# Kernel tuning notes

Hardware: AMD Instinct MI355X
Metric: run time of the kernel (lower is better)

Reference implementation:

```python
import jax, jax.numpy as jnp
import numpy as np
from jax import lax

DN = ('NCHW', 'OIHW', 'NCHW')

def conv(x, w, b, stride):
    y = lax.conv_general_dilated(x, w, (stride, stride), ((1, 1), (1, 1)), dimension_numbers=DN)
    return y + b[None, :, None, None]

def deconv(x, w, b):
    # PyTorch ConvTranspose2d(k=3, stride=2, padding=1, output_padding=1): doubles H, W.
    # w has torch layout [in, out, kH, kW]; convert to OIHW and flip spatially.
    wt = jnp.flip(w, (-2, -1)).transpose(1, 0, 2, 3)
    y = lax.conv_general_dilated(x, wt, (1, 1), ((1, 2), (1, 2)), lhs_dilation=(2, 2), dimension_numbers=DN)
    return y + b[None, :, None, None]


def setup_inputs() -> dict:
    key = jax.random.key(0)
    ks = jax.random.split(key, 16)
    s = 0.05
    d = {
        'x': jax.random.normal(ks[0], (16, 3, 256, 256), jnp.float32),
        'w1': jax.random.normal(ks[1], (64, 3, 3, 3), jnp.float32) * s,
        'b1': jnp.zeros((64,), jnp.float32),
        'w2': jax.random.normal(ks[2], (128, 64, 3, 3), jnp.float32) * s,
        'b2': jnp.zeros((128,), jnp.float32),
        'w3': jax.random.normal(ks[3], (256, 128, 3, 3), jnp.float32) * s,
        'b3': jnp.zeros((256,), jnp.float32),
        'w4': jax.random.normal(ks[4], (512, 256, 3, 3), jnp.float32) * s,
        'b4': jnp.zeros((512,), jnp.float32),
        'codebook': jax.random.normal(ks[5], (8192, 512), jnp.float32),
        # ConvTranspose2d weights in torch layout [in, out, kH, kW]
        'd1w': jax.random.normal(ks[6], (512, 256, 3, 3), jnp.float32) * s,
        'd1b': jnp.zeros((256,), jnp.float32),
        'd2w': jax.random.normal(ks[7], (256, 128, 3, 3), jnp.float32) * s,
        'd2b': jnp.zeros((128,), jnp.float32),
        'd3w': jax.random.normal(ks[8], (128, 64, 3, 3), jnp.float32) * s,
        'd3b': jnp.zeros((64,), jnp.float32),
        'wo': jax.random.normal(ks[9], (3, 64, 3, 3), jnp.float32) * s,
        'bo': jnp.zeros((3,), jnp.float32),
    }
    return d


def reference(x, w1, b1, w2, b2, w3, b3, w4, b4, codebook, d1w, d1b, d2w, d2b, d3w, d3b, wo, bo):
    # Encoder: 256 -> 256 -> 128 -> 64 -> 32 spatial
    h = jax.nn.relu(conv(x, w1, b1, 1))
    h = jax.nn.relu(conv(h, w2, b2, 2))
    h = jax.nn.relu(conv(h, w3, b3, 2))
    z = conv(h, w4, b4, 2)  # [B, 512, 32, 32]

    # Quantize: nearest codebook entry per spatial vector (channels-last).
    B, C, H, W = z.shape
    zf = z.transpose(0, 2, 3, 1).reshape(-1, C)  # [N, 512]
    # squared euclidean distances; argmin identical to cdist argmin
    d2 = (jnp.sum(zf * zf, axis=-1, keepdims=True)
          - 2.0 * (zf @ codebook.T)
          + jnp.sum(codebook * codebook, axis=-1))  # [N, K]
    indices = jnp.argmin(d2, axis=-1)  # [N]
    zq = codebook[indices].reshape(B, H, W, C).transpose(0, 3, 1, 2)  # [B, 512, 32, 32]

    # Decoder: 32 -> 64 -> 128 -> 256
    g = jax.nn.relu(deconv(zq, d1w, d1b))
    g = jax.nn.relu(deconv(g, d2w, d2b))
    g = jax.nn.relu(deconv(g, d3w, d3b))
    x_recon = jax.nn.sigmoid(conv(g, wo, bo, 1))
    return x_recon, indices
```

## Files before the change

kernel.cpp:

```cpp
#include <hip/hip_runtime.h>
#include <cstddef>

typedef short short8 __attribute__((ext_vector_type(8)));
typedef _Float16 half8 __attribute__((ext_vector_type(8)));
typedef _Float16 half4 __attribute__((ext_vector_type(4)));
typedef _Float16 half2v __attribute__((ext_vector_type(2)));
typedef float floatx4 __attribute__((ext_vector_type(4)));

__device__ __forceinline__ unsigned short f2bf(float f) {
    unsigned u = __float_as_uint(f);
    u += 0x7FFFu + ((u >> 16) & 1u);
    return (unsigned short)(u >> 16);
}
__device__ __forceinline__ float bf2f(unsigned short h) {
    return __uint_as_float((unsigned)h << 16);
}

__global__ __launch_bounds__(256)
void fused_conv12_mfma_kernel(const float* __restrict__ x,
                              const float* __restrict__ w1,
                              const float* __restrict__ b1,
                              const _Float16* __restrict__ w2h,
                              const _Float16* __restrict__ w2l,
                              const float* __restrict__ b2,
                              _Float16* __restrict__ outH,
                              _Float16* __restrict__ outL)
{
    __shared__ float s_x[3][11][36];
    __shared__ _Float16 sE[2][9][17][40];
    __shared__ _Float16 sO[2][9][16][40];

    const int tid = threadIdx.x;
    const int lane = tid & 63;
    const int wave = tid >> 6;
    const int n16 = lane & 15;
    const int quad = lane >> 4;

    const int ox0 = (blockIdx.x & 7) * 16;
    const int oy0 = (blockIdx.x >> 3) * 4;
    const int co0 = blockIdx.y * 64 + wave * 16;
    const int img = blockIdx.z;

    const int hy0 = oy0 * 2 - 1, hx0 = ox0 * 2 - 1;
    const int gy0 = hy0 - 1,     gx0 = hx0 - 1;
    const float* xN = x + (size_t)img * 3 * 65536;

    for (int e = tid; e < 3 * 11 * 35; e += 256) {
        int c = e / 385, r = e % 385;
        int yy = r / 35, xx = r % 35;
        int gy = gy0 + yy, gx = gx0 + xx;
        float v = 0.f;
        if ((unsigned)gy < 256u && (unsigned)gx < 256u)
            v = xN[(size_t)c * 65536 + gy * 256 + gx];
        s_x[c][yy][xx] = v;
    }

    floatx4 acc1[4], acc2[4];
#pragma unroll
    for (int s = 0; s < 4; s++) {
        acc1[s] = (floatx4){0.f, 0.f, 0.f, 0.f};
        acc2[s] = (floatx4){0.f, 0.f, 0.f, 0.f};
    }

    const int pair = tid & 15;
    const int pxg  = tid >> 4;

    for (int c0 = 0; c0 < 64; c0 += 32) {
        __syncthreads();

        const int ch0 = c0 + pair * 2;
        float wA[27], wB[27];
#pragma unroll
        for (int k = 0; k < 27; k++) {
            wA[k] = w1[ch0 * 27 + k];
            wB[k] = w1[ch0 * 27 + 27 + k];
        }
        const float bA = b1[ch0], bB = b1[ch0 + 1];

        for (int px = pxg; px < 33; px += 16) {
            const bool colok = (unsigned)(hx0 + px) < 256u;
            float xw[3][3][3];
#pragma unroll
            for (int c = 0; c < 3; c++)
#pragma unroll
                for (int r = 0; r < 3; r++)
#pragma unroll
                    for (int kx = 0; kx < 3; kx++)
                        xw[c][r][kx] = s_x[c][r][px + kx];
#pragma unroll
            for (int py = 0; py < 9; py++) {
                const bool inb = colok && (unsigned)(hy0 + py) < 256u;
                float aA = bA, aB = bB;
#pragma unroll
                for (int c = 0; c < 3; c++)
#pragma unroll
                    for (int k = 0; k < 9; k++) {
                        const float xv = xw[c][k / 3][k % 3];
                        aA += wA[c * 9 + k] * xv;
                        aB += wB[c * 9 + k] * xv;
                    }
                float vA = inb ? fmaxf(aA, 0.f) : 0.f;
                float vB = inb ? fmaxf(aB, 0.f) : 0.f;
                half2v hv, lv;
                _Float16 hA = (_Float16)vA, hB = (_Float16)vB;
                hv[0] = hA; hv[1] = hB;
                lv[0] = (_Float16)((vA - (float)hA) * 1024.f);
                lv[1] = (_Float16)((vB - (float)hB) * 1024.f);
                _Float16* dH = (px & 1) ? &sO[0][py][px >> 1][pair * 2]
                                        : &sE[0][py][px >> 1][pair * 2];
                _Float16* dL = (px & 1) ? &sO[1][py][px >> 1][pair * 2]
                                        : &sE[1][py][px >> 1][pair * 2];
                *(half2v*)dH = hv;
                *(half2v*)dL = lv;
                if (py < 8) {
#pragma unroll
                    for (int c = 0; c < 3; c++) {
#pragma unroll
                        for (int r = 0; r < 2; r++)
#pragma unroll
                            for (int kx = 0; kx < 3; kx++)
                                xw[c][r][kx] = xw[c][r + 1][kx];
#pragma unroll
                        for (int kx = 0; kx < 3; kx++)
                            xw[c][2][kx] = s_x[c][py + 3][px + kx];
                    }
                }
            }
        }
        __syncthreads();

        half8 ah[9], al[9];
#pragma unroll
        for (int tp = 0; tp < 9; tp++) {
            size_t o = ((size_t)(tp * 128 + co0 + n16)) * 64 + c0 + quad * 8;
            ah[tp] = *(const half8*)(w2h + o);
            al[tp] = *(const half8*)(w2l + o);
        }
#pragma unroll
        for (int oy = 0; oy < 4; oy++) {
#pragma unroll
            for (int tp = 0; tp < 9; tp++) {
                const int kx = tp % 3;
                const int row = oy * 2 + tp / 3;
                half8 bh, bl;
                if (kx == 0)      { bh = *(const half8*)&sE[0][row][n16][quad * 8];
                                    bl = *(const half8*)&sE[1][row][n16][quad * 8]; }
                else if (kx == 1) { bh = *(const half8*)&sO[0][row][n16][quad * 8];
                                    bl = *(const half8*)&sO[1][row][n16][quad * 8]; }
                else              { bh = *(const half8*)&sE[0][row][n16 + 1][quad * 8];
                                    bl = *(const half8*)&sE[1][row][n16 + 1][quad * 8]; }
                acc1[oy] = __builtin_amdgcn_mfma_f32_16x16x32_f16(ah[tp], bh, acc1[oy], 0, 0, 0);
                acc2[oy] = __builtin_amdgcn_mfma_f32_16x16x32_f16(ah[tp], bl, acc2[oy], 0, 0, 0);
                acc2[oy] = __builtin_amdgcn_mfma_f32_16x16x32_f16(al[tp], bh, acc2[oy], 0, 0, 0);
            }
        }
    }

    const float4 bv = *(const float4*)&b2[co0 + quad * 4];
    const float bb[4] = {bv.x, bv.y, bv.z, bv.w};
#pragma unroll
    for (int oy = 0; oy < 4; oy++) {
        half4 hv, lv;
#pragma unroll
        for (int r = 0; r < 4; r++) {
            float v = fmaxf(acc1[oy][r] + acc2[oy][r] * (1.0f / 1024.0f) + bb[r], 0.f);
            _Float16 h = (_Float16)v;
            hv[r] = h;
            lv[r] = (_Float16)((v - (float)h) * 1024.f);
        }
        size_t o = (((size_t)img * 128 + (oy0 + oy)) * 128 + (ox0 + n16)) * 128
                   + co0 + quad * 4;
        *(half4*)(outH + o) = hv;
        *(half4*)(outL + o) = lv;
    }
}

template<int CI, int CO>
__global__ __launch_bounds__(256)
void prepack_conv_kernel(const float* __restrict__ w,
                         _Float16* __restrict__ wh, _Float16* __restrict__ wl)
{
    int i = blockIdx.x * 256 + threadIdx.x;
    if (i >= CO * CI * 9) return;
    int co = i / (CI * 9);
    int r  = i % (CI * 9);
    int ci = r / 9;
    int tp = r % 9;
    float v = w[i];
    _Float16 h = (_Float16)v;
    size_t o = ((size_t)tp * CO + co) * CI + ci;
    wh[o] = h;
    wl[o] = (_Float16)((v - (float)h) * 1024.f);
}

template<int CIN, int COUT, int IH, int IW, bool RELU>
__global__ __launch_bounds__(256)
void conv_mfma_kernel(const _Float16* __restrict__ inH, const _Float16* __restrict__ inL,
                      const _Float16* __restrict__ wpH, const _Float16* __restrict__ wpL,
                      const float* __restrict__ bias,
                      _Float16* __restrict__ outH, _Float16* __restrict__ outL)
{
    constexpr int OH = IH / 2, OW = IW / 2;
    __shared__ _Float16 sE[2][9][17][40];
    __shared__ _Float16 sO[2][9][16][40];

    const int tid = threadIdx.x;
    const int lane = tid & 63;
    const int wave = tid >> 6;
    const int n16 = lane & 15;
    const int quad = lane >> 4;

    constexpr int NTX = OW / 16;
    const int ox0 = (blockIdx.x % NTX) * 16;
    const int oy0 = (blockIdx.x / NTX) * 4;
    const int co0 = blockIdx.y * 64 + wave * 16;
    const int img = blockIdx.z;

    const int iy0 = oy0 * 2 - 1;
    const int ix0 = ox0 * 2 - 1;
    const _Float16* iNH = inH + (size_t)img * IH * IW * CIN;
    const _Float16* iNL = inL + (size_t)img * IH * IW * CIN;

    floatx4 acc1[4], acc2[4];
#pragma unroll
    for (int s = 0; s < 4; s++) {
        acc1[s] = (floatx4){0.f, 0.f, 0.f, 0.f};
        acc2[s] = (floatx4){0.f, 0.f, 0.f, 0.f};
    }

    for (int k0 = 0; k0 < CIN; k0 += 32) {
        __syncthreads();
        for (int e = tid; e < 2376; e += 256) {
            int pl = e / 1188;
            int r  = e % 1188;
            int pix = r >> 2, q = r & 3;
            int py = pix / 33, px = pix % 33;
            int iy = iy0 + py, ix = ix0 + px;
            half8 v = (half8)(_Float16)0;
            if ((unsigned)iy < (unsigned)IH && (unsigned)ix < (unsigned)IW)
                v = *(const half8*)((pl ? iNL : iNH) + ((size_t)(iy * IW + ix) * CIN + k0 + q * 8));
            if (px & 1) *(half8*)&sO[pl][py][px >> 1][q * 8] = v;
            else        *(half8*)&sE[pl][py][px >> 1][q * 8] = v;
        }
        __syncthreads();

        half8 ah[9], al[9];
#pragma unroll
        for (int tp = 0; tp < 9; tp++) {
            size_t o = ((size_t)(tp * COUT + co0 + n16)) * CIN + k0 + quad * 8;
            ah[tp] = *(const half8*)(wpH + o);
            al[tp] = *(const half8*)(wpL + o);
        }

#pragma unroll
        for (int oy = 0; oy < 4; oy++) {
#pragma unroll
            for (int tp = 0; tp < 9; tp++) {
                const int ky = tp / 3, kx = tp % 3;
                const int row = oy * 2 + ky;
                half8 bh, bl;
                if (kx == 0)      { bh = *(const half8*)&sE[0][row][n16][quad * 8];
                                    bl = *(const half8*)&sE[1][row][n16][quad * 8]; }
                else if (kx == 1) { bh = *(const half8*)&sO[0][row][n16][quad * 8];
                                    bl = *(const half8*)&sO[1][row][n16][quad * 8]; }
                else              { bh = *(const half8*)&sE[0][row][n16 + 1][quad * 8];
                                    bl = *(const half8*)&sE[1][row][n16 + 1][quad * 8]; }
                acc1[oy] = __builtin_amdgcn_mfma_f32_16x16x32_f16(ah[tp], bh, acc1[oy], 0, 0, 0);
                acc2[oy] = __builtin_amdgcn_mfma_f32_16x16x32_f16(ah[tp], bl, acc2[oy], 0, 0, 0);
                acc2[oy] = __builtin_amdgcn_mfma_f32_16x16x32_f16(al[tp], bh, acc2[oy], 0, 0, 0);
            }
        }
    }

    const float4 bv = *(const float4*)&bias[co0 + quad * 4];
    const float bb[4] = {bv.x, bv.y, bv.z, bv.w};
#pragma unroll
    for (int oy = 0; oy < 4; oy++) {
        half4 hv, lv;
#pragma unroll
        for (int r = 0; r < 4; r++) {
            float v = acc1[oy][r] + acc2[oy][r] * (1.0f / 1024.0f) + bb[r];
            if (RELU) v = fmaxf(v, 0.f);
            _Float16 h = (_Float16)v;
            hv[r] = h;
            lv[r] = (_Float16)((v - (float)h) * 1024.f);
        }
        size_t o = (((size_t)img * OH + (oy0 + oy)) * OW + (ox0 + n16)) * COUT
                   + co0 + quad * 4;
        *(half4*)(outH + o) = hv;
        *(half4*)(outL + o) = lv;
    }
}

__global__ __launch_bounds__(64)
void cnorm_kernel(const float* __restrict__ cb, float* __restrict__ cn)
{
    const int code = blockIdx.x;
    const int t = threadIdx.x;
    const float* row = cb + (size_t)code * 512;
    float s = 0.f;
    for (int i = t; i < 512; i += 64) s += row[i] * row[i];
#pragma unroll
    for (int off = 32; off > 0; off >>= 1) s += __shfl_down(s, off, 64);
    if (t == 0) cn[code] = s;
}

__global__ __launch_bounds__(256)
void init_keys_kernel(unsigned long long* __restrict__ keys)
{
    keys[blockIdx.x * 256 + threadIdx.x] = ~0ull;
}

__global__ __launch_bounds__(256)
void split_cb_kernel(const float* __restrict__ cb,
                     _Float16* __restrict__ ch, _Float16* __restrict__ cl)
{
    size_t i = (size_t)blockIdx.x * 256 + threadIdx.x;
    float v = cb[i];
    _Float16 h = (_Float16)v;
    ch[i] = h;
    cl[i] = (_Float16)((v - (float)h) * 1024.f);
}

__global__ __launch_bounds__(256)
void vq_mfma_kernel(const _Float16* __restrict__ zh, const _Float16* __restrict__ zl,
                    const _Float16* __restrict__ ch, const _Float16* __restrict__ cl,
                    const float* __restrict__ cn,
                    unsigned long long* __restrict__ keys)
{
    __shared__ _Float16 sB[2][512 * 8];

    const int tid = threadIdx.x;
    const int lane = tid & 63;
    const int wave = tid >> 6;
    const int n16 = lane & 15;
    const int quad = lane >> 4;

    const int code0 = blockIdx.x * 64;
    const int row0 = blockIdx.y * 128 + wave * 32;

    floatx4 acc1[2][4], acc2[2][4];
#pragma unroll
    for (int rt = 0; rt < 2; rt++)
#pragma unroll
        for (int ct = 0; ct < 4; ct++) {
            acc1[rt][ct] = (floatx4){0.f, 0.f, 0.f, 0.f};
            acc2[rt][ct] = (floatx4){0.f, 0.f, 0.f, 0.f};
        }

    const _Float16* pzh = zh + (size_t)(row0 + n16) * 512 + quad * 8;
    const _Float16* pzl = zl + (size_t)(row0 + n16) * 512 + quad * 8;

    const _Float16* s0 = ch
        + (size_t)(code0 + ((tid >> 6) & 3) * 16 + (tid & 15)) * 512 + ((tid >> 4) & 3) * 8;
    const _Float16* s1 = cl
        + (size_t)(code0 + ((tid >> 6) & 3) * 16 + (tid & 15)) * 512 + ((tid >> 4) & 3) * 8;

    half8 As[2][4];
    As[0][0] = *(const half8*)(pzh);
    As[0][1] = *(const half8*)(pzh + 8192);
    As[0][2] = *(const half8*)(pzl);
    As[0][3] = *(const half8*)(pzl + 8192);
    *(half8*)&sB[0][tid * 8]         = *(const half8*)s0;
    *(half8*)&sB[0][(tid + 256) * 8] = *(const half8*)s1;
    __syncthreads();

    for (int c = 0; c < 16; ++c) {
        const int cur = c & 1;
        const int kk = c * 32;
        half8 t0, t1;
        if (c < 15) {
            const int nxt = cur ^ 1;
            As[nxt][0] = *(const half8*)(pzh + kk + 32);
            As[nxt][1] = *(const half8*)(pzh + 8192 + kk + 32);
            As[nxt][2] = *(const half8*)(pzl + kk + 32);
            As[nxt][3] = *(const half8*)(pzl + 8192 + kk + 32);
            t0 = *(const half8*)(s0 + kk + 32);
            t1 = *(const half8*)(s1 + kk + 32);
        }
#pragma unroll
        for (int ct = 0; ct < 4; ++ct) {
            half8 bh = *(const half8*)&sB[cur][(ct * 64 + lane) * 8];
            half8 bl = *(const half8*)&sB[cur][((4 + ct) * 64 + lane) * 8];
#pragma unroll
            for (int rt = 0; rt < 2; rt++) {
                acc1[rt][ct] = __builtin_amdgcn_mfma_f32_16x16x32_f16(As[cur][rt],     bh, acc1[rt][ct], 0, 0, 0);
                acc2[rt][ct] = __builtin_amdgcn_mfma_f32_16x16x32_f16(As[cur][rt],     bl, acc2[rt][ct], 0, 0, 0);
                acc2[rt][ct] = __builtin_amdgcn_mfma_f32_16x16x32_f16(As[cur][2 + rt], bh, acc2[rt][ct], 0, 0, 0);
            }
        }
        if (c < 15) {
            const int nxt = cur ^ 1;
            *(half8*)&sB[nxt][tid * 8]         = t0;
            *(half8*)&sB[nxt][(tid + 256) * 8] = t1;
        }
        __syncthreads();
    }

#pragma unroll
    for (int rt = 0; rt < 2; rt++) {
#pragma unroll
        for (int reg = 0; reg < 4; reg++) {
            float best = 3.0e38f;
            int bcode = 0;
#pragma unroll
            for (int ct = 0; ct < 4; ct++) {
                const int code = code0 + ct * 16 + n16;
                float dot = acc1[rt][ct][reg] + acc2[rt][ct][reg] * (1.0f / 1024.0f);
                float s = cn[code] - 2.0f * dot;
                if (s < best) { best = s; bcode = code; }
            }
            unsigned u = __float_as_uint(best);
            u = (u & 0x80000000u) ? ~u : (u | 0x80000000u);
            unsigned long long key = ((unsigned long long)u << 32) | (unsigned)bcode;
#pragma unroll
            for (int m = 1; m < 16; m <<= 1) {
                unsigned long long o = __shfl_xor(key, m, 64);
                key = (o < key) ? o : key;
            }
            if (n16 == 0)
                atomicMin(&keys[row0 + rt * 16 + quad * 4 + reg], key);
        }
    }
}

__global__ __launch_bounds__(256)
void vq_gather_kernel(const unsigned long long* __restrict__ keys,
                      const float* __restrict__ cb,
                      unsigned short* __restrict__ zq, float* __restrict__ idx_out)
{
    __shared__ int sidx[64];
    const int t = threadIdx.x;
    const int v0 = blockIdx.x * 64;
    if (t < 64) {
        int idx = (int)(keys[v0 + t] & 0xFFFFFFFFull);
        sidx[t] = idx;
        idx_out[v0 + t] = (float)idx;
    }
    __syncthreads();
    const int tv = t >> 2;
    const int q = t & 3;
    const float* crow = cb + (size_t)sidx[tv] * 512;
    unsigned short* zrow = zq + (size_t)(v0 + tv) * 512;
    for (int c = q * 8; c < 512; c += 32) {
        float4 f0 = *(const float4*)(crow + c);
        float4 f1 = *(const float4*)(crow + c + 4);
        short8 h;
        h[0] = (short)f2bf(f0.x); h[1] = (short)f2bf(f0.y);
        h[2] = (short)f2bf(f0.z); h[3] = (short)f2bf(f0.w);
        h[4] = (short)f2bf(f1.x); h[5] = (short)f2bf(f1.y);
        h[6] = (short)f2bf(f1.z); h[7] = (short)f2bf(f1.w);
        *(short8*)(zrow + c) = h;
    }
}

template<int CI, int CO>
__global__ __launch_bounds__(256)
void prepack_kernel(const float* __restrict__ w, unsigned short* __restrict__ wp)
{
    int i = blockIdx.x * 256 + threadIdx.x;
    if (i >= 9 * CO * CI) return;
    int ci = i / (CO * 9);
    int r  = i % (CO * 9);
    int co = r / 9;
    int tp = r % 9;
    wp[((size_t)tp * CO + co) * CI + ci] = f2bf(w[i]);
}

template<int CIN, int COUT, int IH, int IW, bool OUT_NCHW>
__global__ __launch_bounds__(256)
void deconv_mfma_kernel(const unsigned short* __restrict__ in,
                        const unsigned short* __restrict__ wp,
                        const float* __restrict__ bias,
                        unsigned short* __restrict__ out)
{
    constexpr int OH = 2 * IH, OW = 2 * IW;
    __shared__ short sIn[5][17][40];

    const int tid = threadIdx.x;
    const int lane = tid & 63;
    const int wave = tid >> 6;
    const int n16 = lane & 15;
    const int quad = lane >> 4;

    constexpr int NTX = IW / 16;
    const int x0 = (blockIdx.x % NTX) * 16;
    const int y0 = (blockIdx.x / NTX) * 4;
    const int co0 = blockIdx.y * 64 + wave * 16;
    const int img = blockIdx.z;

    const unsigned short* inN = in + (size_t)img * IH * IW * CIN;

    floatx4 acc[4][4];
#pragma unroll
    for (int s = 0; s < 4; s++)
#pragma unroll
        for (int c = 0; c < 4; c++) acc[s][c] = (floatx4){0.f, 0.f, 0.f, 0.f};

    for (int k0 = 0; k0 < CIN; k0 += 32) {
        __syncthreads();
        for (int e = tid; e < 340; e += 256) {
            int yy = e / 68, r = e % 68;
            int xx = r >> 2, q4 = r & 3;
            int gy = y0 + yy, gx = x0 + xx;
            short8 v = {0, 0, 0, 0, 0, 0, 0, 0};
            if (gy < IH && gx < IW)
                v = *(const short8*)(inN + ((size_t)(gy * IW + gx) * CIN + k0 + q4 * 8));
            *(short8*)&sIn[yy][xx][q4 * 8] = v;
        }
        __syncthreads();

        short8 a[9];
#pragma unroll
        for (int tp = 0; tp < 9; tp++)
            a[tp] = *(const short8*)(wp + ((size_t)(tp * COUT + co0 + n16) * CIN + k0 + quad * 8));

#pragma unroll
        for (int s = 0; s < 4; s++) {
            short8 b00 = *(const short8*)&sIn[s    ][n16    ][quad * 8];
            short8 b01 = *(const short8*)&sIn[s    ][n16 + 1][quad * 8];
            short8 b10 = *(const short8*)&sIn[s + 1][n16    ][quad * 8];
            short8 b11 = *(const short8*)&sIn[s + 1][n16 + 1][quad * 8];
            acc[s][0] = __builtin_amdgcn_mfma_f32_16x16x32_bf16(a[4], b00, acc[s][0], 0, 0, 0);
            acc[s][1] = __builtin_amdgcn_mfma_f32_16x16x32_bf16(a[3], b01, acc[s][1], 0, 0, 0);
            acc[s][1] = __builtin_amdgcn_mfma_f32_16x16x32_bf16(a[5], b00, acc[s][1], 0, 0, 0);
            acc[s][2] = __builtin_amdgcn_mfma_f32_16x16x32_bf16(a[1], b10, acc[s][2], 0, 0, 0);
            acc[s][2] = __builtin_amdgcn_mfma_f32_16x16x32_bf16(a[7], b00, acc[s][2], 0, 0, 0);
            acc[s][3] = __builtin_amdgcn_mfma_f32_16x16x32_bf16(a[0], b11, acc[s][3], 0, 0, 0);
            acc[s][3] = __builtin_amdgcn_mfma_f32_16x16x32_bf16(a[2], b10, acc[s][3], 0, 0, 0);
            acc[s][3] = __builtin_amdgcn_mfma_f32_16x16x32_bf16(a[6], b01, acc[s][3], 0, 0, 0);
            acc[s][3] = __builtin_amdgcn_mfma_f32_16x16x32_bf16(a[8], b00, acc[s][3], 0, 0, 0);
        }
    }

    const float4 bv = *(const float4*)&bias[co0 + quad * 4];
    const float bb[4] = {bv.x, bv.y, bv.z, bv.w};
    const int x = x0 + n16;

    if (!OUT_NCHW) {
        unsigned short* outN = out + (size_t)img * OH * OW * COUT;
#pragma unroll
        for (int s = 0; s < 4; s++) {
            const int y = y0 + s;
#pragma unroll
            for (int c = 0; c < 4; c++) {
                const int oy = 2 * y + (c >> 1);
                const int ox = 2 * x + (c & 1);
                ushort4 h;
                h.x = f2bf(fmaxf(acc[s][c][0] + bb[0], 0.f));
                h.y = f2bf(fmaxf(acc[s][c][1] + bb[1], 0.f));
                h.z = f2bf(fmaxf(acc[s][c][2] + bb[2], 0.f));
                h.w = f2bf(fmaxf(acc[s][c][3] + bb[3], 0.f));
                *(ushort4*)(outN + ((size_t)(oy * OW + ox) * COUT + co0 + quad * 4)) = h;
            }
        }
    } else {
#pragma unroll
        for (int s = 0; s < 4; s++) {
            const int y = y0 + s;
#pragma unroll
            for (int r = 0; r < 4; r++) {
                const int co = co0 + quad * 4 + r;
                unsigned short* oC = out + (size_t)(img * COUT + co) * OH * OW;
                unsigned p0 = (unsigned)f2bf(fmaxf(acc[s][0][r] + bb[r], 0.f)) |
                              ((unsigned)f2bf(fmaxf(acc[s][1][r] + bb[r], 0.f)) << 16);
                unsigned p1 = (unsigned)f2bf(fmaxf(acc[s][2][r] + bb[r], 0.f)) |
                              ((unsigned)f2bf(fmaxf(acc[s][3][r] + bb[r], 0.f)) << 16);
                *(unsigned*)(oC + (size_t)(2 * y) * OW + 2 * x) = p0;
                *(unsigned*)(oC + (size_t)(2 * y + 1) * OW + 2 * x) = p1;
            }
        }
    }
}

__global__ __launch_bounds__(256)
void conv_out_kernel(const unsigned short* __restrict__ in,
                     const float* __restrict__ w,
                     const float* __restrict__ bias,
                     float* __restrict__ out)
{
    constexpr int TIC = 4;
    __shared__ float s_in[TIC][3][258];
    const int t = threadIdx.x;
    const int y = blockIdx.x;
    const int n = blockIdx.y;
    const unsigned short* inN = in + (size_t)n * 64 * 65536;
    float acc0 = bias[0], acc1 = bias[1], acc2 = bias[2];

    for (int c0 = 0; c0 < 64; c0 += TIC) {
        for (int e = t; e < TIC * 3 * 258; e += 256) {
            int ci = e / 774;
            int r  = e % 774;
            int ry = r / 258, xx = r % 258;
            int gy = y - 1 + ry, gx = xx - 1;
            float v = 0.f;
            if ((unsigned)gy < 256u && (unsigned)gx < 256u)
                v = bf2f(inN[(size_t)(c0 + ci) * 65536 + gy * 256 + gx]);
            s_in[ci][ry][xx] = v;
        }
        __syncthreads();
#pragma unroll
        for (int ci = 0; ci < TIC; ++ci) {
            float iv[3][3];
#pragma unroll
            for (int ry = 0; ry < 3; ry++)
#pragma unroll
                for (int kx = 0; kx < 3; kx++)
                    iv[ry][kx] = s_in[ci][ry][t + kx];
#pragma unroll
            for (int k = 0; k < 9; k++) {
                const float v = iv[k / 3][k % 3];
                acc0 += w[(0 * 64 + c0 + ci) * 9 + k] * v;
                acc1 += w[(1 * 64 + c0 + ci) * 9 + k] * v;
                acc2 += w[(2 * 64 + c0 + ci) * 9 + k] * v;
            }
        }
        __syncthreads();
    }
    const size_t o = (size_t)((n * 3 + 0) * 256 + y) * 256 + t;
    out[o]          = 1.f / (1.f + __expf(-acc0));
    out[o + 65536]  = 1.f / (1.f + __expf(-acc1));
    out[o + 131072] = 1.f / (1.f + __expf(-acc2));
}

extern "C" void kernel_launch(void* const* d_in, const int* in_sizes, int n_in,
                              void* d_out, int out_size, void* d_ws, size_t ws_size,
                              hipStream_t stream)
{
    const float* x   = (const float*)d_in[0];
    const float* w1  = (const float*)d_in[1];
    const float* b1  = (const float*)d_in[2];
    const float* w2  = (const float*)d_in[3];
    const float* b2  = (const float*)d_in[4];
    const float* w3  = (const float*)d_in[5];
    const float* b3  = (const float*)d_in[6];
    const float* w4  = (const float*)d_in[7];
    const float* b4  = (const float*)d_in[8];
    const float* cb  = (const float*)d_in[9];
    const float* d1w = (const float*)d_in[10];
    const float* d1b = (const float*)d_in[11];
    const float* d2w = (const float*)d_in[12];
    const float* d2b = (const float*)d_in[13];
    const float* d3w = (const float*)d_in[14];
    const float* d3b = (const float*)d_in[15];
    const float* wo  = (const float*)d_in[16];
    const float* bo  = (const float*)d_in[17];

    char* ws = (char*)d_ws;
    _Float16* H2H = (_Float16*)(ws);
    _Float16* H2L = (_Float16*)(ws + 67108864);
    _Float16* H3H = (_Float16*)(ws + 134217728);
    _Float16* H3L = (_Float16*)(ws + 167772160);
    _Float16* ZH  = (_Float16*)(ws);
    _Float16* ZL  = (_Float16*)(ws + 16777216);
    unsigned short* ZQ = (unsigned short*)(ws + 33554432);
    _Float16* CBH = (_Float16*)(ws + 50331648);
    _Float16* CBL = (_Float16*)(ws + 58720256);
    unsigned short* G1 = (unsigned short*)(ws + 67108864);
    unsigned short* G2 = (unsigned short*)(ws + 134217728);
    unsigned short* G3 = (unsigned short*)(ws);
    unsigned long long* keys = (unsigned long long*)(ws + 201326592);
    float* cn = (float*)(ws + 201326592 + 131072);

    char* oscratch = (char*)d_out;
    _Float16* EW3H = (_Float16*)(oscratch);
    _Float16* EW3L = (_Float16*)(oscratch + 589824);
    _Float16* EW4H = (_Float16*)(oscratch + 1179648);
    _Float16* EW4L = (_Float16*)(oscratch + 3538944);
    unsigned short* WP1 = (unsigned short*)(oscratch + 5898240);
    unsigned short* WP2 = (unsigned short*)(oscratch + 8257536);
    unsigned short* WP3 = (unsigned short*)(oscratch + 8847360);
    _Float16* EW2H = (_Float16*)(oscratch + 8994816);
    _Float16* EW2L = (_Float16*)(oscratch + 9142272);

    float* xrec = (float*)d_out;
    float* idxf = (float*)d_out + (size_t)16 * 3 * 256 * 256;

    prepack_conv_kernel<64,  128><<<288,  256, 0, stream>>>(w2, EW2H, EW2L);
    prepack_conv_kernel<128, 256><<<1152, 256, 0, stream>>>(w3, EW3H, EW3L);
    prepack_conv_kernel<256, 512><<<4608, 256, 0, stream>>>(w4, EW4H, EW4L);
    prepack_kernel<512, 256><<<4608, 256, 0, stream>>>(d1w, WP1);
    prepack_kernel<256, 128><<<1152, 256, 0, stream>>>(d2w, WP2);
    prepack_kernel<128, 64 ><<<288,  256, 0, stream>>>(d3w, WP3);

    fused_conv12_mfma_kernel<<<dim3(256, 2, 16), 256, 0, stream>>>(x, w1, b1, EW2H, EW2L, b2, H2H, H2L);
    conv_mfma_kernel<128, 256, 128, 128, true ><<<dim3(64, 4, 16), 256, 0, stream>>>(H2H, H2L, EW3H, EW3L, b3, H3H, H3L);
    conv_mfma_kernel<256, 512, 64,  64,  false><<<dim3(16, 8, 16), 256, 0, stream>>>(H3H, H3L, EW4H, EW4L, b4, ZH, ZL);

    cnorm_kernel<<<8192, 64, 0, stream>>>(cb, cn);
    init_keys_kernel<<<64, 256, 0, stream>>>(keys);
    split_cb_kernel<<<16384, 256, 0, stream>>>(cb, CBH, CBL);
    vq_mfma_kernel<<<dim3(128, 128), 256, 0, stream>>>(ZH, ZL, CBH, CBL, cn, keys);
    vq_gather_kernel<<<256, 256, 0, stream>>>(keys, cb, ZQ, idxf);

    deconv_mfma_kernel<512, 256, 32,  32,  false><<<dim3(16,  4, 16), 256, 0, stream>>>(ZQ, WP1, d1b, G1);
    deconv_mfma_kernel<256, 128, 64,  64,  false><<<dim3(64,  2, 16), 256, 0, stream>>>(G1, WP2, d2b, G2);
    deconv_mfma_kernel<128, 64,  128, 128, true ><<<dim3(256, 1, 16), 256, 0, stream>>>(G2, WP3, d3b, G3);
    conv_out_kernel<<<dim3(256, 16), 256, 0, stream>>>(G3, wo, bo, xrec);
}
```

Measured before the change: 2.310 ms.

## Double K-step per VQ iteration and swizzle block order for L2 reuse

The VQ distance kernel now stages 64 K-elements of codebook per shared-memory buffer instead of 32, which halves the number of loop iterations and barriers. A-operand fragments are loaded directly each iteration rather than software-prefetched. Block indices are remapped so groups of 16 row tiles sweep all code tiles together, aiming to improve L2 reuse of z rows and codebook tiles. This doubles shared memory per block, which may reduce occupancy, and the A loads are no longer overlapped with compute.

```diff
diff --git a/kernel.cpp b/kernel.cpp
--- a/kernel.cpp
+++ b/kernel.cpp
@@ -328,7 +328,7 @@
                     const float* __restrict__ cn,
                     unsigned long long* __restrict__ keys)
 {
-    __shared__ _Float16 sB[2][512 * 8];
+    __shared__ _Float16 sB[2][1024 * 8];
 
     const int tid = threadIdx.x;
     const int lane = tid & 63;
@@ -336,8 +336,11 @@
     const int n16 = lane & 15;
     const int quad = lane >> 4;
 
-    const int code0 = blockIdx.x * 64;
-    const int row0 = blockIdx.y * 128 + wave * 32;
+    const int bid = blockIdx.y * 128 + blockIdx.x;
+    const int grp = bid >> 11;
+    const int r   = bid & 2047;
+    const int code0 = (r >> 4) * 64;
+    const int row0 = (grp * 16 + (r & 15)) * 128 + wave * 32;
 
     floatx4 acc1[2][4], acc2[2][4];
 #pragma unroll
@@ -351,48 +354,58 @@
     const _Float16* pzh = zh + (size_t)(row0 + n16) * 512 + quad * 8;
     const _Float16* pzl = zl + (size_t)(row0 + n16) * 512 + quad * 8;
 
-    const _Float16* s0 = ch
-        + (size_t)(code0 + ((tid >> 6) & 3) * 16 + (tid & 15)) * 512 + ((tid >> 4) & 3) * 8;
-    const _Float16* s1 = cl
-        + (size_t)(code0 + ((tid >> 6) & 3) * 16 + (tid & 15)) * 512 + ((tid >> 4) & 3) * 8;
-
-    half8 As[2][4];
-    As[0][0] = *(const half8*)(pzh);
-    As[0][1] = *(const half8*)(pzh + 8192);
-    As[0][2] = *(const half8*)(pzl);
-    As[0][3] = *(const half8*)(pzl + 8192);
-    *(half8*)&sB[0][tid * 8]         = *(const half8*)s0;
-    *(half8*)&sB[0][(tid + 256) * 8] = *(const half8*)s1;
+    const _Float16* bs[4];
+#pragma unroll
+    for (int j = 0; j < 4; j++) {
+        const int e = tid + j * 256;
+        const int pl = e >> 9, ks = (e >> 8) & 1, ct = (e >> 6) & 3;
+        const int l = e & 63;
+        bs[j] = (pl ? cl : ch)
+              + (size_t)(code0 + ct * 16 + (l & 15)) * 512 + ks * 32 + (l >> 4) * 8;
+    }
+
+#pragma unroll
+    for (int j = 0; j < 4; j++)
+        *(half8*)&sB[0][(tid + j * 256) * 8] = *(const half8*)(bs[j]);
     __syncthreads();
 
-    for (int c = 0; c < 16; ++c) {
+    for (int c = 0; c < 8; ++c) {
         const int cur = c & 1;
-        const int kk = c * 32;
-        half8 t0, t1;
-        if (c < 15) {
+        const int kb = c * 64;
+        half8 t[4];
+        if (c < 7) {
+#pragma unroll
+            for (int j = 0; j < 4; j++)
+                t[j] = *(const half8*)(bs[j] + kb + 64);
+        }
+        half8 ah[2][2], al[2][2];
+#pragma unroll
+        for (int rt = 0; rt < 2; rt++)
+#pragma unroll
+            for (int ks = 0; ks < 2; ks++) {
+                ah[rt][ks] = *(const half8*)(pzh + rt * 8192 + kb + ks * 32);
+                al[rt][ks] = *(const half8*)(pzl + rt * 8192 + kb + ks * 32);
+            }
+#pragma unroll
+        for (int ks = 0; ks < 2; ks++) {
+#pragma unroll
+            for (int ct = 0; ct < 4; ++ct) {
+                const int fb = (ks * 4 + ct) * 64 + lane;
+                half8 bh = *(const half8*)&sB[cur][fb * 8];
+                half8 bl = *(const half8*)&sB[cur][(fb + 512) * 8];
+#pragma unroll
+                for (int rt = 0; rt < 2; rt++) {
+                    acc1[rt][ct] = __builtin_amdgcn_mfma_f32_16x16x32_f16(ah[rt][ks], bh, acc1[rt][ct], 0, 0, 0);
+                    acc2[rt][ct] = __builtin_amdgcn_mfma_f32_16x16x32_f16(ah[rt][ks], bl, acc2[rt][ct], 0, 0, 0);
+                    acc2[rt][ct] = __builtin_amdgcn_mfma_f32_16x16x32_f16(al[rt][ks], bh, acc2[rt][ct], 0, 0, 0);
+                }
+            }
+        }
+        if (c < 7) {
             const int nxt = cur ^ 1;
-            As[nxt][0] = *(const half8*)(pzh + kk + 32);
-            As[nxt][1] = *(const half8*)(pzh + 8192 + kk + 32);
-            As[nxt][2] = *(const half8*)(pzl + kk + 32);
-            As[nxt][3] = *(const half8*)(pzl + 8192 + kk + 32);
-            t0 = *(const half8*)(s0 + kk + 32);
-            t1 = *(const half8*)(s1 + kk + 32);
-        }
-#pragma unroll
-        for (int ct = 0; ct < 4; ++ct) {
-            half8 bh = *(const half8*)&sB[cur][(ct * 64 + lane) * 8];
-            half8 bl = *(const half8*)&sB[cur][((4 + ct) * 64 + lane) * 8];
-#pragma unroll
-            for (int rt = 0; rt < 2; rt++) {
-                acc1[rt][ct] = __builtin_amdgcn_mfma_f32_16x16x32_f16(As[cur][rt],     bh, acc1[rt][ct], 0, 0, 0);
-                acc2[rt][ct] = __builtin_amdgcn_mfma_f32_16x16x32_f16(As[cur][rt],     bl, acc2[rt][ct], 0, 0, 0);
-                acc2[rt][ct] = __builtin_amdgcn_mfma_f32_16x16x32_f16(As[cur][2 + rt], bh, acc2[rt][ct], 0, 0, 0);
-            }
-        }
-        if (c < 15) {
-            const int nxt = cur ^ 1;
-            *(half8*)&sB[nxt][tid * 8]         = t0;
-            *(half8*)&sB[nxt][(tid + 256) * 8] = t1;
+#pragma unroll
+            for (int j = 0; j < 4; j++)
+                *(half8*)&sB[nxt][(tid + j * 256) * 8] = t[j];
         }
         __syncthreads();
     }
```

Result: no change. 2.314 ms (+0.2%).
